# Performance work log

Measured on AMD Instinct MI355X. Metric: run time of the kernel, lower is better.

## Reference

```python
import jax, jax.numpy as jnp
import numpy as np

N_NODES = 100000
N_EDGES = 1600000
N_FEAT = 64
HIDDEN = 64
N_GRAPHS = 256


def setup_inputs() -> dict:
    key = jax.random.key(0)
    ks = jax.random.split(key, 8)
    x = jax.random.normal(ks[0], (N_NODES, N_FEAT), dtype=jnp.float32)
    edge_index = jax.random.randint(ks[1], (2, N_EDGES), 0, N_NODES, dtype=jnp.int64)
    batch = jnp.sort(jax.random.randint(ks[2], (N_NODES,), 0, N_GRAPHS, dtype=jnp.int64))
    W1 = jax.random.normal(ks[3], (N_FEAT, HIDDEN), dtype=jnp.float32) / np.sqrt(N_FEAT)
    b1 = jnp.zeros((HIDDEN,), dtype=jnp.float32)
    W2 = jax.random.normal(ks[4], (HIDDEN, HIDDEN), dtype=jnp.float32) / np.sqrt(HIDDEN)
    b2 = jnp.zeros((HIDDEN,), dtype=jnp.float32)
    Wfc = jax.random.normal(ks[5], (HIDDEN, 1), dtype=jnp.float32) / np.sqrt(HIDDEN)
    bfc = jnp.zeros((1,), dtype=jnp.float32)
    return {"x": x, "edge_index": edge_index, "batch": batch,
            "W1": W1, "b1": b1, "W2": W2, "b2": b2, "Wfc": Wfc, "bfc": bfc}


def _gcn_conv(x, W, b, src, dst, norm, n_nodes):
    # h = X W, then symmetric-normalized scatter-add aggregation at dst
    h = x @ W  # [N, H]
    msg = h[src] * norm[:, None]  # [E+N, H] gather + scale
    agg = jax.ops.segment_sum(msg, dst, num_segments=n_nodes)
    return agg + b


def reference(x, edge_index, batch, W1, b1, W2, b2, Wfc, bfc):
    n = x.shape[0]
    loops = jnp.arange(n, dtype=edge_index.dtype)
    src = jnp.concatenate([edge_index[0], loops])  # add self-loops (GCNConv default)
    dst = jnp.concatenate([edge_index[1], loops])
    deg = jax.ops.segment_sum(jnp.ones_like(dst, dtype=x.dtype), dst, num_segments=n)
    dinv = jnp.where(deg > 0, jax.lax.rsqrt(deg), 0.0)
    norm = dinv[src] * dinv[dst]  # D^-1/2 (A+I) D^-1/2

    h = jax.nn.relu(_gcn_conv(x, W1, b1, src, dst, norm, n))  # dropout = identity (eval)
    h = jax.nn.relu(_gcn_conv(h, W2, b2, src, dst, norm, n))

    # global mean pool over graphs
    sums = jax.ops.segment_sum(h, batch, num_segments=N_GRAPHS)
    counts = jax.ops.segment_sum(jnp.ones((n,), dtype=h.dtype), batch, num_segments=N_GRAPHS)
    pooled = sums / jnp.maximum(counts, 1.0)[:, None]  # [G, H]
    return jax.nn.sigmoid(pooled @ Wfc + bfc)  # [G, 1]
```

## Files before the change

kernel.cpp:

```cpp
#include <hip/hip_runtime.h>
#include <hip/hip_fp16.h>
#include <math.h>

#define N_NODES  100000
#define N_EDGES  1600000
#define NF       64
#define N_GRAPHS 256
#define SRC_SPLIT 50000

#define BSH   7
#define NB    ((N_NODES + 127) / 128)
#define BCAP  2600

typedef float f32x2 __attribute__((ext_vector_type(2)));

__global__ void k_zerocur(int* __restrict__ bucketCur, float* __restrict__ gsum,
                          int* __restrict__ Ah8, int* __restrict__ Ah8b) {
    int i = blockIdx.x * blockDim.x + threadIdx.x;
    if (i < NB) bucketCur[i] = 0;
    if (i < N_GRAPHS) gsum[i] = 0.0f;
    if (i < 16) {
        Ah8 [(size_t)N_NODES * 16 + i] = 0;
        Ah8b[(size_t)N_NODES * 16 + i] = 0;
    }
}

__global__ __launch_bounds__(1024) void k_bscatter(const int* __restrict__ src,
                                                   const int* __restrict__ dst,
                                                   int* __restrict__ bucketCur,
                                                   int* __restrict__ scratch) {
    __shared__ int hist[NB];
    __shared__ int bbase[NB];
    int t = threadIdx.x;
    for (int i = t; i < NB; i += 1024) hist[i] = 0;
    __syncthreads();
    int e0 = (blockIdx.x * 1024 + t) * 8;
    int d[8], s[8], r[8];
    bool act = (e0 + 7) < N_EDGES;
    if (act) {
        *(int4*)&d[0] = *(const int4*)(dst + e0);
        *(int4*)&d[4] = *(const int4*)(dst + e0 + 4);
        *(int4*)&s[0] = *(const int4*)(src + e0);
        *(int4*)&s[4] = *(const int4*)(src + e0 + 4);
#pragma unroll
        for (int k = 0; k < 8; ++k) r[k] = atomicAdd(&hist[d[k] >> BSH], 1);
    }
    __syncthreads();
    for (int i = t; i < NB; i += 1024)
        if (hist[i]) bbase[i] = atomicAdd(&bucketCur[i], hist[i]);
    __syncthreads();
    if (act) {
#pragma unroll
        for (int k = 0; k < 8; ++k) {
            int b = d[k] >> BSH;
            int pos = bbase[b] + r[k];
            if (pos < BCAP)
                scratch[b * BCAP + pos] = ((d[k] & 127) << 17) | s[k];
        }
    }
}

__global__ __launch_bounds__(1024) void k_bscan(const int* __restrict__ bucketCur,
                                                int* __restrict__ bucketPtr,
                                                int* __restrict__ rowptr) {
    int t = threadIdx.x;
    __shared__ int ps[1024];
    int v = (t < NB) ? min(bucketCur[t], BCAP) : 0;
    ps[t] = v;
    __syncthreads();
#pragma unroll
    for (int off = 1; off < 1024; off <<= 1) {
        int u = (t >= off) ? ps[t - off] : 0;
        __syncthreads();
        ps[t] += u;
        __syncthreads();
    }
    if (t < NB) bucketPtr[t] = ps[t] - v;
    if (t == NB - 1) {
        bucketPtr[NB] = ps[t];
        rowptr[N_NODES] = ps[t];
    }
}

__global__ __launch_bounds__(256) void k_bfinal(const int* __restrict__ bucketCur,
                                                const int* __restrict__ bucketPtr,
                                                const int* __restrict__ scratch,
                                                int* __restrict__ rowptr,
                                                int* __restrict__ rowmid,
                                                float* __restrict__ dinv,
                                                int* __restrict__ col) {
    int b = blockIdx.x;
    int cnt  = min(bucketCur[b], BCAP);
    int base = bucketPtr[b];
    int node0 = b << BSH;
    __shared__ int hist[256];
    __shared__ int escan[256];
    __shared__ int ps[256];
    __shared__ int rnk[BCAP];
    int t = threadIdx.x;
    hist[t] = 0;
    __syncthreads();
    const int* sp = scratch + b * BCAP;
    for (int j = t; j < cnt; j += 256) {
        int pk = sp[j];
        int idx = ((pk >> 17) << 1) | ((pk & 0x1FFFF) >= SRC_SPLIT);
        rnk[j] = atomicAdd(&hist[idx], 1);
    }
    __syncthreads();
    int hv = hist[t];
    ps[t] = hv;
    __syncthreads();
#pragma unroll
    for (int off = 1; off < 256; off <<= 1) {
        int u = (t >= off) ? ps[t - off] : 0;
        __syncthreads();
        ps[t] += u;
        __syncthreads();
    }
    escan[t] = ps[t] - hv;
    __syncthreads();
    if (t < 128) {
        int node = node0 + t;
        if (node < N_NODES) {
            int cL = hist[t * 2], cH = hist[t * 2 + 1];
            rowptr[node] = base + escan[t * 2];
            rowmid[node] = base + escan[t * 2 + 1];
            dinv[node] = rsqrtf((float)(cL + cH + 1));
        }
    }
    for (int j = t; j < cnt; j += 256) {
        int pk = sp[j];
        int s = pk & 0x1FFFF;
        int idx = ((pk >> 17) << 1) | (s >= SRC_SPLIT);
        col[base + escan[idx] + rnk[j]] = s;
    }
}

__device__ __forceinline__ void agg_half(const int* __restrict__ cp, int cnt,
                                         const int* __restrict__ Ah8, int oct,
                                         int c[8],
                                         f32x2& a0, f32x2& a1, f32x2& a2, f32x2& a3) {
    for (int base = 0; base < cnt; base += 8) {
        int2 rr[8];
#pragma unroll
        for (int p = 0; p < 8; ++p)
            rr[p] = *(const int2*)(Ah8 + (size_t)c[p] * 16 + oct * 2);
        int nb = base + 8;
#pragma unroll
        for (int p = 0; p < 8; ++p) {
            int v = cp[nb + p];
            c[p] = (nb + p < cnt) ? v : N_NODES;
        }
#pragma unroll
        for (int p = 0; p < 8; ++p) {
            a0 += __builtin_amdgcn_cvt_pk_f32_fp8(rr[p].x, false);
            a1 += __builtin_amdgcn_cvt_pk_f32_fp8(rr[p].x, true);
            a2 += __builtin_amdgcn_cvt_pk_f32_fp8(rr[p].y, false);
            a3 += __builtin_amdgcn_cvt_pk_f32_fp8(rr[p].y, true);
        }
    }
}

__device__ __forceinline__ void agg2(const int* __restrict__ rowptr,
                                     const int* __restrict__ rowmid,
                                     const int* __restrict__ col,
                                     const int* __restrict__ Ah8,
                                     int n, int oct,
                                     f32x2& a0, f32x2& a1, f32x2& a2, f32x2& a3) {
    int nn  = (n < N_NODES) ? n : N_NODES;
    int beg = 0, mid = 0, end = 0;
    if (n < N_NODES) { beg = rowptr[n]; mid = rowmid[n]; end = rowptr[n + 1]; }
    int cntL = mid - beg, cntH = end - mid;
    {
        int2 raw = *(const int2*)(Ah8 + (size_t)nn * 16 + oct * 2);
        a0 += __builtin_amdgcn_cvt_pk_f32_fp8(raw.x, false);
        a1 += __builtin_amdgcn_cvt_pk_f32_fp8(raw.x, true);
        a2 += __builtin_amdgcn_cvt_pk_f32_fp8(raw.y, false);
        a3 += __builtin_amdgcn_cvt_pk_f32_fp8(raw.y, true);
    }
    const int* cpL = col + beg;
    const int* cpH = col + mid;
    int cl[8], ch[8];
#pragma unroll
    for (int p = 0; p < 8; ++p) {
        int vl = cpL[p];
        int vh = cpH[p];
        cl[p] = (p < cntL) ? vl : N_NODES;
        ch[p] = (p < cntH) ? vh : N_NODES;
    }
    agg_half(cpL, cntL, Ah8, oct, cl, a0, a1, a2, a3);
    agg_half(cpH, cntH, Ah8, oct, ch, a0, a1, a2, a3);
}

__global__ __launch_bounds__(256) void k_gemm(const float* __restrict__ X,
                                              const float* __restrict__ W,
                                              const float* __restrict__ dinv,
                                              int* __restrict__ Ah8) {
    __shared__ float Ws[64][64];
    __shared__ float Xs[64][68];
    int t  = threadIdx.x;
    int n0 = blockIdx.x * 64;

    for (int i = t; i < 64 * 64; i += 256) Ws[i >> 6][i & 63] = W[i];

#pragma unroll
    for (int p = 0; p < 4; ++p) {
        int flat = p * 256 + t;
        int nl = flat >> 4;
        int kg = flat & 15;
        int node = n0 + nl;
        float4 v = make_float4(0.f, 0.f, 0.f, 0.f);
        if (node < N_NODES)
            v = *(const float4*)(X + (size_t)node * NF + kg * 4);
        Xs[kg * 4 + 0][nl] = v.x;
        Xs[kg * 4 + 1][nl] = v.y;
        Xs[kg * 4 + 2][nl] = v.z;
        Xs[kg * 4 + 3][nl] = v.w;
    }
    __syncthreads();

    int tx = t & 15;
    int ty = t >> 4;
    float acc[4][4];
#pragma unroll
    for (int i = 0; i < 4; ++i)
#pragma unroll
        for (int j = 0; j < 4; ++j) acc[i][j] = 0.f;

#pragma unroll 8
    for (int k = 0; k < 64; ++k) {
        float4 wv = *(const float4*)&Ws[k][tx * 4];
        float4 xv = *(const float4*)&Xs[k][ty * 4];
        acc[0][0] += xv.x * wv.x; acc[0][1] += xv.x * wv.y;
        acc[0][2] += xv.x * wv.z; acc[0][3] += xv.x * wv.w;
        acc[1][0] += xv.y * wv.x; acc[1][1] += xv.y * wv.y;
        acc[1][2] += xv.y * wv.z; acc[1][3] += xv.y * wv.w;
        acc[2][0] += xv.z * wv.x; acc[2][1] += xv.z * wv.y;
        acc[2][2] += xv.z * wv.z; acc[2][3] += xv.z * wv.w;
        acc[3][0] += xv.w * wv.x; acc[3][1] += xv.w * wv.y;
        acc[3][2] += xv.w * wv.z; acc[3][3] += xv.w * wv.w;
    }

#pragma unroll
    for (int i = 0; i < 4; ++i) {
        int node = n0 + ty * 4 + i;
        if (node < N_NODES) {
            float dv = dinv[node];
            int pk = 0;
            pk = __builtin_amdgcn_cvt_pk_fp8_f32(acc[i][0] * dv, acc[i][1] * dv, pk, false);
            pk = __builtin_amdgcn_cvt_pk_fp8_f32(acc[i][2] * dv, acc[i][3] * dv, pk, true);
            Ah8[(size_t)node * 16 + tx] = pk;
        }
    }
}

__global__ __launch_bounds__(256) void k_pullgemm(const int* __restrict__ rowptr,
                                                  const int* __restrict__ rowmid,
                                                  const int* __restrict__ col,
                                                  const float* __restrict__ dinv,
                                                  const int* __restrict__ Ah8,
                                                  const float* __restrict__ W,
                                                  const float* __restrict__ bias,
                                                  int* __restrict__ AhOut) {
    __shared__ float Ws[64][64];
    __shared__ float Xs[64][68];
    int t  = threadIdx.x;
    int n0 = blockIdx.x * 64;

    for (int i = t; i < 64 * 64; i += 256) Ws[i >> 6][i & 63] = W[i];

    int wv      = t >> 6;
    int lane    = t & 63;
    int nodeSub = lane >> 3;
    int oct     = lane & 7;

    float4 bA = *(const float4*)(bias + oct * 8);
    float4 bB = *(const float4*)(bias + oct * 8 + 4);

#pragma unroll
    for (int r = 0; r < 2; ++r) {
        int nl = wv * 16 + r * 8 + nodeSub;
        int n  = n0 + nl;
        f32x2 a0 = {0.f, 0.f}, a1 = {0.f, 0.f}, a2 = {0.f, 0.f}, a3 = {0.f, 0.f};
        agg2(rowptr, rowmid, col, Ah8, n, oct, a0, a1, a2, a3);
        float dv = (n < N_NODES) ? dinv[n] : 0.f;
        float f0 = a0.x * dv + bA.x; Xs[oct * 8 + 0][nl] = f0 > 0.f ? f0 : 0.f;
        float f1 = a0.y * dv + bA.y; Xs[oct * 8 + 1][nl] = f1 > 0.f ? f1 : 0.f;
        float f2 = a1.x * dv + bA.z; Xs[oct * 8 + 2][nl] = f2 > 0.f ? f2 : 0.f;
        float f3 = a1.y * dv + bA.w; Xs[oct * 8 + 3][nl] = f3 > 0.f ? f3 : 0.f;
        float f4 = a2.x * dv + bB.x; Xs[oct * 8 + 4][nl] = f4 > 0.f ? f4 : 0.f;
        float f5 = a2.y * dv + bB.y; Xs[oct * 8 + 5][nl] = f5 > 0.f ? f5 : 0.f;
        float f6 = a3.x * dv + bB.z; Xs[oct * 8 + 6][nl] = f6 > 0.f ? f6 : 0.f;
        float f7 = a3.y * dv + bB.w; Xs[oct * 8 + 7][nl] = f7 > 0.f ? f7 : 0.f;
    }
    __syncthreads();

    int tx = t & 15;
    int ty = t >> 4;
    float acc[4][4];
#pragma unroll
    for (int i = 0; i < 4; ++i)
#pragma unroll
        for (int j = 0; j < 4; ++j) acc[i][j] = 0.f;

#pragma unroll 8
    for (int k = 0; k < 64; ++k) {
        float4 wvv = *(const float4*)&Ws[k][tx * 4];
        float4 xv  = *(const float4*)&Xs[k][ty * 4];
        acc[0][0] += xv.x * wvv.x; acc[0][1] += xv.x * wvv.y;
        acc[0][2] += xv.x * wvv.z; acc[0][3] += xv.x * wvv.w;
        acc[1][0] += xv.y * wvv.x; acc[1][1] += xv.y * wvv.y;
        acc[1][2] += xv.y * wvv.z; acc[1][3] += xv.y * wvv.w;
        acc[2][0] += xv.z * wvv.x; acc[2][1] += xv.z * wvv.y;
        acc[2][2] += xv.z * wvv.z; acc[2][3] += xv.z * wvv.w;
        acc[3][0] += xv.w * wvv.x; acc[3][1] += xv.w * wvv.y;
        acc[3][2] += xv.w * wvv.z; acc[3][3] += xv.w * wvv.w;
    }

#pragma unroll
    for (int i = 0; i < 4; ++i) {
        int node = n0 + ty * 4 + i;
        if (node < N_NODES) {
            float dv = dinv[node];
            int pk = 0;
            pk = __builtin_amdgcn_cvt_pk_fp8_f32(acc[i][0] * dv, acc[i][1] * dv, pk, false);
            pk = __builtin_amdgcn_cvt_pk_fp8_f32(acc[i][2] * dv, acc[i][3] * dv, pk, true);
            AhOut[(size_t)node * 16 + tx] = pk;
        }
    }
}

__global__ __launch_bounds__(256) void k_pullpool(const int* __restrict__ rowptr,
                                                  const int* __restrict__ rowmid,
                                                  const int* __restrict__ col,
                                                  const float* __restrict__ dinv,
                                                  const int* __restrict__ Ah8,
                                                  const float* __restrict__ b2,
                                                  const float* __restrict__ Wfc,
                                                  const int* __restrict__ batch,
                                                  float* __restrict__ gsum) {
    int t       = threadIdx.x;
    int lane    = t & 63;
    int wv      = t >> 6;
    int nodeSub = lane >> 3;
    int oct     = lane & 7;
    int n = blockIdx.x * 32 + wv * 8 + nodeSub;

    float4 bA = *(const float4*)(b2 + oct * 8);
    float4 bB = *(const float4*)(b2 + oct * 8 + 4);
    float4 wA = *(const float4*)(Wfc + oct * 8);
    float4 wB = *(const float4*)(Wfc + oct * 8 + 4);

    f32x2 a0 = {0.f, 0.f}, a1 = {0.f, 0.f}, a2 = {0.f, 0.f}, a3 = {0.f, 0.f};
    agg2(rowptr, rowmid, col, Ah8, n, oct, a0, a1, a2, a3);

    int   g  = (n < N_NODES) ? (int)batch[n] : -1;
    float dv = (n < N_NODES) ? dinv[n] : 0.f;

    float wsum = 0.f;
    float v;
    v = a0.x * dv + bA.x; wsum += (v > 0.f ? v : 0.f) * wA.x;
    v = a0.y * dv + bA.y; wsum += (v > 0.f ? v : 0.f) * wA.y;
    v = a1.x * dv + bA.z; wsum += (v > 0.f ? v : 0.f) * wA.z;
    v = a1.y * dv + bA.w; wsum += (v > 0.f ? v : 0.f) * wA.w;
    v = a2.x * dv + bB.x; wsum += (v > 0.f ? v : 0.f) * wB.x;
    v = a2.y * dv + bB.y; wsum += (v > 0.f ? v : 0.f) * wB.y;
    v = a3.x * dv + bB.z; wsum += (v > 0.f ? v : 0.f) * wB.z;
    v = a3.y * dv + bB.w; wsum += (v > 0.f ? v : 0.f) * wB.w;
    wsum += __shfl_xor(wsum, 1);
    wsum += __shfl_xor(wsum, 2);
    wsum += __shfl_xor(wsum, 4);

    float sv = (oct == 0) ? wsum : 0.f;
    int   gv = (oct == 0) ? g : -2;
#pragma unroll
    for (int off = 8; off < 64; off <<= 1) {
        float s2 = __shfl_down(sv, off);
        int   g2 = __shfl_down(gv, off);
        if (g2 == gv) sv += s2;
    }
    int gp = __shfl_up(gv, 8);
    bool head = (lane < 8) || (gp != gv);
    if (oct == 0 && g >= 0 && head) atomicAdd(&gsum[g], sv);
}

__device__ __forceinline__ int lower_bound_i(const int* __restrict__ a, int n, int key) {
    int lo = 0, hi = n;
    while (lo < hi) {
        int mid = (lo + hi) >> 1;
        if (a[mid] < key) lo = mid + 1; else hi = mid;
    }
    return lo;
}

__global__ void k_final(const int* __restrict__ batch,
                        const float* __restrict__ gsum,
                        const float* __restrict__ bfc,
                        float* __restrict__ out) {
    int g = blockIdx.x * blockDim.x + threadIdx.x;
    if (g < N_GRAPHS) {
        int lo = lower_bound_i(batch, N_NODES, g);
        int hi = lower_bound_i(batch, N_NODES, g + 1);
        float c = (hi > lo) ? (float)(hi - lo) : 1.0f;
        float v = gsum[g] / c + bfc[0];
        out[g] = 1.0f / (1.0f + expf(-v));
    }
}

extern "C" void kernel_launch(void* const* d_in, const int* in_sizes, int n_in,
                              void* d_out, int out_size, void* d_ws, size_t ws_size,
                              hipStream_t stream) {
    const float* x    = (const float*)d_in[0];
    const int*   ei   = (const int*)d_in[1];
    const int*   batch= (const int*)d_in[2];
    const float* W1   = (const float*)d_in[3];
    const float* b1   = (const float*)d_in[4];
    const float* W2   = (const float*)d_in[5];
    const float* b2   = (const float*)d_in[6];
    const float* Wfc  = (const float*)d_in[7];
    const float* bfc  = (const float*)d_in[8];
    float* out = (float*)d_out;

    const int* src = ei;
    const int* dst = ei + N_EDGES;

    int*    Ah8       = (int*)d_ws;
    int*    Ah8b      = Ah8 + (size_t)(N_NODES + 1) * 16;
    float*  dinv      = (float*)(Ah8b + (size_t)(N_NODES + 1) * 16);
    int*    rowptr    = (int*)(dinv + N_NODES);
    int*    rowmid    = rowptr + N_NODES + 1;
    int*    bucketCur = rowmid + N_NODES;
    int*    bucketPtr = bucketCur + NB;
    int*    col       = bucketPtr + NB + 1;
    float*  gsum      = (float*)(col + N_EDGES);
    int*    scratch   = (int*)(gsum + N_GRAPHS);

    const int BLK = 256;
    int g_gemm = (N_NODES + 63) / 64;
    int g_pp   = (N_NODES + 31) / 32;
    int g_bsc  = (N_EDGES / 8 + 1023) / 1024;

    k_zerocur<<<(NB + BLK - 1) / BLK, BLK, 0, stream>>>(bucketCur, gsum, Ah8, Ah8b);
    k_bscatter<<<g_bsc, 1024, 0, stream>>>(src, dst, bucketCur, scratch);
    k_bscan<<<1, 1024, 0, stream>>>(bucketCur, bucketPtr, rowptr);
    k_bfinal<<<NB, BLK, 0, stream>>>(bucketCur, bucketPtr, scratch, rowptr, rowmid, dinv, col);

    k_gemm<<<g_gemm, BLK, 0, stream>>>(x, W1, dinv, Ah8);

    k_pullgemm<<<g_gemm, BLK, 0, stream>>>(rowptr, rowmid, col, dinv, Ah8, W2, b1, Ah8b);

    k_pullpool<<<g_pp, BLK, 0, stream>>>(rowptr, rowmid, col, dinv, Ah8b, b2, Wfc, batch, gsum);
    k_final<<<1, BLK, 0, stream>>>(batch, gsum, bfc, out);
}
```

Baseline: 238.3 us.

## Split each aggregation pass by source half to keep gathered features cache-resident

Measured after the change: 255.3 us. +7.2%, slower.

```diff
diff --git a/kernel.cpp b/kernel.cpp
--- a/kernel.cpp
+++ b/kernel.cpp
@@ -13,6 +13,7 @@
 #define BCAP  2600
 
 typedef float f32x2 __attribute__((ext_vector_type(2)));
+typedef int   i32x4 __attribute__((ext_vector_type(4)));
 
 __global__ void k_zerocur(int* __restrict__ bucketCur, float* __restrict__ gsum,
                           int* __restrict__ Ah8, int* __restrict__ Ah8b) {
@@ -136,10 +137,24 @@
     }
 }
 
+__device__ __forceinline__ void gat1(const int* __restrict__ Ah8, int idx, int oct,
+                                     f32x2& a0, f32x2& a1, f32x2& a2, f32x2& a3) {
+    int2 raw = *(const int2*)(Ah8 + (size_t)idx * 16 + oct * 2);
+    a0 += __builtin_amdgcn_cvt_pk_f32_fp8(raw.x, false);
+    a1 += __builtin_amdgcn_cvt_pk_f32_fp8(raw.x, true);
+    a2 += __builtin_amdgcn_cvt_pk_f32_fp8(raw.y, false);
+    a3 += __builtin_amdgcn_cvt_pk_f32_fp8(raw.y, true);
+}
+
 __device__ __forceinline__ void agg_half(const int* __restrict__ cp, int cnt,
                                          const int* __restrict__ Ah8, int oct,
-                                         int c[8],
                                          f32x2& a0, f32x2& a1, f32x2& a2, f32x2& a3) {
+    int c[8];
+#pragma unroll
+    for (int p = 0; p < 8; ++p) {
+        int v = __builtin_nontemporal_load(cp + p);
+        c[p] = (p < cnt) ? v : N_NODES;
+    }
     for (int base = 0; base < cnt; base += 8) {
         int2 rr[8];
 #pragma unroll
@@ -148,7 +163,7 @@
         int nb = base + 8;
 #pragma unroll
         for (int p = 0; p < 8; ++p) {
-            int v = cp[nb + p];
+            int v = __builtin_nontemporal_load(cp + nb + p);
             c[p] = (nb + p < cnt) ? v : N_NODES;
         }
 #pragma unroll
@@ -161,35 +176,11 @@
     }
 }
 
-__device__ __forceinline__ void agg2(const int* __restrict__ rowptr,
-                                     const int* __restrict__ rowmid,
-                                     const int* __restrict__ col,
-                                     const int* __restrict__ Ah8,
-                                     int n, int oct,
-                                     f32x2& a0, f32x2& a1, f32x2& a2, f32x2& a3) {
-    int nn  = (n < N_NODES) ? n : N_NODES;
-    int beg = 0, mid = 0, end = 0;
-    if (n < N_NODES) { beg = rowptr[n]; mid = rowmid[n]; end = rowptr[n + 1]; }
-    int cntL = mid - beg, cntH = end - mid;
-    {
-        int2 raw = *(const int2*)(Ah8 + (size_t)nn * 16 + oct * 2);
-        a0 += __builtin_amdgcn_cvt_pk_f32_fp8(raw.x, false);
-        a1 += __builtin_amdgcn_cvt_pk_f32_fp8(raw.x, true);
-        a2 += __builtin_amdgcn_cvt_pk_f32_fp8(raw.y, false);
-        a3 += __builtin_amdgcn_cvt_pk_f32_fp8(raw.y, true);
-    }
-    const int* cpL = col + beg;
-    const int* cpH = col + mid;
-    int cl[8], ch[8];
-#pragma unroll
-    for (int p = 0; p < 8; ++p) {
-        int vl = cpL[p];
-        int vh = cpH[p];
-        cl[p] = (p < cntL) ? vl : N_NODES;
-        ch[p] = (p < cntH) ? vh : N_NODES;
-    }
-    agg_half(cpL, cntL, Ah8, oct, cl, a0, a1, a2, a3);
-    agg_half(cpH, cntH, Ah8, oct, ch, a0, a1, a2, a3);
+__device__ __forceinline__ int h2_to_i(__half2 h) {
+    int i; __builtin_memcpy(&i, &h, 4); return i;
+}
+__device__ __forceinline__ float2 i_to_f2(int i) {
+    __half2 h; __builtin_memcpy(&h, &i, 4); return __half22float2(h);
 }
 
 __global__ __launch_bounds__(256) void k_gemm(const float* __restrict__ X,
@@ -254,14 +245,42 @@
     }
 }
 
-__global__ __launch_bounds__(256) void k_pullgemm(const int* __restrict__ rowptr,
-                                                  const int* __restrict__ rowmid,
-                                                  const int* __restrict__ col,
-                                                  const float* __restrict__ dinv,
-                                                  const int* __restrict__ Ah8,
-                                                  const float* __restrict__ W,
-                                                  const float* __restrict__ bias,
-                                                  int* __restrict__ AhOut) {
+__global__ __launch_bounds__(256) void k_pull_lo(const int* __restrict__ rowptr,
+                                                 const int* __restrict__ rowmid,
+                                                 const int* __restrict__ col,
+                                                 const int* __restrict__ Ah8,
+                                                 int* __restrict__ P) {
+    int t       = threadIdx.x;
+    int lane    = t & 63;
+    int wv      = t >> 6;
+    int nodeSub = lane >> 3;
+    int oct     = lane & 7;
+    int n = blockIdx.x * 32 + wv * 8 + nodeSub;
+    if (n >= N_NODES) return;
+
+    f32x2 a0 = {0.f, 0.f}, a1 = {0.f, 0.f}, a2 = {0.f, 0.f}, a3 = {0.f, 0.f};
+    int beg = rowptr[n];
+    int mid = rowmid[n];
+    if (n < SRC_SPLIT) gat1(Ah8, n, oct, a0, a1, a2, a3);
+    agg_half(col + beg, mid - beg, Ah8, oct, a0, a1, a2, a3);
+
+    i32x4 pv;
+    pv.x = h2_to_i(__floats2half2_rn(a0.x, a0.y));
+    pv.y = h2_to_i(__floats2half2_rn(a1.x, a1.y));
+    pv.z = h2_to_i(__floats2half2_rn(a2.x, a2.y));
+    pv.w = h2_to_i(__floats2half2_rn(a3.x, a3.y));
+    __builtin_nontemporal_store(pv, (i32x4*)(P + (size_t)n * 32 + oct * 4));
+}
+
+__global__ __launch_bounds__(256) void k_pullgemm_hi(const int* __restrict__ rowptr,
+                                                     const int* __restrict__ rowmid,
+                                                     const int* __restrict__ col,
+                                                     const float* __restrict__ dinv,
+                                                     const int* __restrict__ Ah8,
+                                                     const int* __restrict__ P,
+                                                     const float* __restrict__ W,
+                                                     const float* __restrict__ bias,
+                                                     int* __restrict__ AhOut) {
     __shared__ float Ws[64][64];
     __shared__ float Xs[64][68];
     int t  = threadIdx.x;
@@ -282,16 +301,31 @@
         int nl = wv * 16 + r * 8 + nodeSub;
         int n  = n0 + nl;
         f32x2 a0 = {0.f, 0.f}, a1 = {0.f, 0.f}, a2 = {0.f, 0.f}, a3 = {0.f, 0.f};
-        agg2(rowptr, rowmid, col, Ah8, n, oct, a0, a1, a2, a3);
-        float dv = (n < N_NODES) ? dinv[n] : 0.f;
-        float f0 = a0.x * dv + bA.x; Xs[oct * 8 + 0][nl] = f0 > 0.f ? f0 : 0.f;
-        float f1 = a0.y * dv + bA.y; Xs[oct * 8 + 1][nl] = f1 > 0.f ? f1 : 0.f;
-        float f2 = a1.x * dv + bA.z; Xs[oct * 8 + 2][nl] = f2 > 0.f ? f2 : 0.f;
-        float f3 = a1.y * dv + bA.w; Xs[oct * 8 + 3][nl] = f3 > 0.f ? f3 : 0.f;
-        float f4 = a2.x * dv + bB.x; Xs[oct * 8 + 4][nl] = f4 > 0.f ? f4 : 0.f;
-        float f5 = a2.y * dv + bB.y; Xs[oct * 8 + 5][nl] = f5 > 0.f ? f5 : 0.f;
-        float f6 = a3.x * dv + bB.z; Xs[oct * 8 + 6][nl] = f6 > 0.f ? f6 : 0.f;
-        float f7 = a3.y * dv + bB.w; Xs[oct * 8 + 7][nl] = f7 > 0.f ? f7 : 0.f;
+        float dv = 0.f;
+        i32x4 pv = {0, 0, 0, 0};
+        bool valid = (n < N_NODES);
+        if (valid) {
+            pv = __builtin_nontemporal_load((const i32x4*)(P + (size_t)n * 32 + oct * 4));
+            int mid = rowmid[n];
+            int end = rowptr[n + 1];
+            if (n >= SRC_SPLIT) gat1(Ah8, n, oct, a0, a1, a2, a3);
+            agg_half(col + mid, end - mid, Ah8, oct, a0, a1, a2, a3);
+            dv = dinv[n];
+        }
+        float2 f0 = i_to_f2(pv.x), f1 = i_to_f2(pv.y);
+        float2 f2 = i_to_f2(pv.z), f3 = i_to_f2(pv.w);
+        a0.x += f0.x; a0.y += f0.y;
+        a1.x += f1.x; a1.y += f1.y;
+        a2.x += f2.x; a2.y += f2.y;
+        a3.x += f3.x; a3.y += f3.y;
+        float g0 = a0.x * dv + bA.x; Xs[oct * 8 + 0][nl] = g0 > 0.f ? g0 : 0.f;
+        float g1 = a0.y * dv + bA.y; Xs[oct * 8 + 1][nl] = g1 > 0.f ? g1 : 0.f;
+        float g2 = a1.x * dv + bA.z; Xs[oct * 8 + 2][nl] = g2 > 0.f ? g2 : 0.f;
+        float g3 = a1.y * dv + bA.w; Xs[oct * 8 + 3][nl] = g3 > 0.f ? g3 : 0.f;
+        float g4 = a2.x * dv + bB.x; Xs[oct * 8 + 4][nl] = g4 > 0.f ? g4 : 0.f;
+        float g5 = a2.y * dv + bB.y; Xs[oct * 8 + 5][nl] = g5 > 0.f ? g5 : 0.f;
+        float g6 = a3.x * dv + bB.z; Xs[oct * 8 + 6][nl] = g6 > 0.f ? g6 : 0.f;
+        float g7 = a3.y * dv + bB.w; Xs[oct * 8 + 7][nl] = g7 > 0.f ? g7 : 0.f;
     }
     __syncthreads();
 
@@ -330,15 +364,16 @@
     }
 }
 
-__global__ __launch_bounds__(256) void k_pullpool(const int* __restrict__ rowptr,
-                                                  const int* __restrict__ rowmid,
-                                                  const int* __restrict__ col,
-                                                  const float* __restrict__ dinv,
-                                                  const int* __restrict__ Ah8,
-                                                  const float* __restrict__ b2,
-                                                  const float* __restrict__ Wfc,
-                                                  const int* __restrict__ batch,
-                                                  float* __restrict__ gsum) {
+__global__ __launch_bounds__(256) void k_pullpool_hi(const int* __restrict__ rowptr,
+                                                     const int* __restrict__ rowmid,
+                                                     const int* __restrict__ col,
+                                                     const float* __restrict__ dinv,
+                                                     const int* __restrict__ Ah8,
+                                                     const int* __restrict__ P,
+                                                     const float* __restrict__ b2,
+                                                     const float* __restrict__ Wfc,
+                                                     const int* __restrict__ batch,
+                                                     float* __restrict__ gsum) {
     int t       = threadIdx.x;
     int lane    = t & 63;
     int wv      = t >> 6;
@@ -352,10 +387,24 @@
     float4 wB = *(const float4*)(Wfc + oct * 8 + 4);
 
     f32x2 a0 = {0.f, 0.f}, a1 = {0.f, 0.f}, a2 = {0.f, 0.f}, a3 = {0.f, 0.f};
-    agg2(rowptr, rowmid, col, Ah8, n, oct, a0, a1, a2, a3);
-
-    int   g  = (n < N_NODES) ? (int)batch[n] : -1;
-    float dv = (n < N_NODES) ? dinv[n] : 0.f;
+    float dv = 0.f;
+    int   g  = -1;
+    i32x4 pv = {0, 0, 0, 0};
+    if (n < N_NODES) {
+        pv = __builtin_nontemporal_load((const i32x4*)(P + (size_t)n * 32 + oct * 4));
+        int mid = rowmid[n];
+        int end = rowptr[n + 1];
+        if (n >= SRC_SPLIT) gat1(Ah8, n, oct, a0, a1, a2, a3);
+        agg_half(col + mid, end - mid, Ah8, oct, a0, a1, a2, a3);
+        dv = dinv[n];
+        g  = batch[n];
+    }
+    float2 f0 = i_to_f2(pv.x), f1 = i_to_f2(pv.y);
+    float2 f2 = i_to_f2(pv.z), f3 = i_to_f2(pv.w);
+    a0.x += f0.x; a0.y += f0.y;
+    a1.x += f1.x; a1.y += f1.y;
+    a2.x += f2.x; a2.y += f2.y;
+    a3.x += f3.x; a3.y += f3.y;
 
     float wsum = 0.f;
     float v;
@@ -371,7 +420,7 @@
     wsum += __shfl_xor(wsum, 2);
     wsum += __shfl_xor(wsum, 4);
 
-    float sv = (oct == 0) ? wsum : 0.f;
+    float sv = (oct == 0 && n < N_NODES) ? wsum : 0.f;
     int   gv = (oct == 0) ? g : -2;
 #pragma unroll
     for (int off = 8; off < 64; off <<= 1) {
@@ -434,6 +483,7 @@
     int*    col       = bucketPtr + NB + 1;
     float*  gsum      = (float*)(col + N_EDGES);
     int*    scratch   = (int*)(gsum + N_GRAPHS);
+    int*    P         = scratch + (size_t)NB * BCAP;
 
     const int BLK = 256;
     int g_gemm = (N_NODES + 63) / 64;
@@ -447,8 +497,10 @@
 
     k_gemm<<<g_gemm, BLK, 0, stream>>>(x, W1, dinv, Ah8);
 
-    k_pullgemm<<<g_gemm, BLK, 0, stream>>>(rowptr, rowmid, col, dinv, Ah8, W2, b1, Ah8b);
-
-    k_pullpool<<<g_pp, BLK, 0, stream>>>(rowptr, rowmid, col, dinv, Ah8b, b2, Wfc, batch, gsum);
+    k_pull_lo<<<g_pp, BLK, 0, stream>>>(rowptr, rowmid, col, Ah8, P);
+    k_pullgemm_hi<<<g_gemm, BLK, 0, stream>>>(rowptr, rowmid, col, dinv, Ah8, P, W2, b1, Ah8b);
+
+    k_pull_lo<<<g_pp, BLK, 0, stream>>>(rowptr, rowmid, col, Ah8b, P);
+    k_pullpool_hi<<<g_pp, BLK, 0, stream>>>(rowptr, rowmid, col, dinv, Ah8b, P, b2, Wfc, batch, gsum);
     k_final<<<1, BLK, 0, stream>>>(batch, gsum, bfc, out);
 }
```
